# Optimization experiments

Hardware: AMD Instinct MI355X
Metric: run time of the kernel (lower is better)

Reference implementation:

```python
import jax, jax.numpy as jnp
import numpy as np

B = 4            # batches in the sparse tensor
N_PER = 250_000  # occupied voxels per batch item
L = 200          # voxel grid extent per axis
C = 64           # in_channels == out_channels (SE block forces equality)
K = 27           # 3x3x3 kernel offsets
BN_EPS = 1e-5


def _build_neighbors():
    """Unique random voxel coords per batch; kernel map [27, N] (-1 = missing)."""
    rng = np.random.default_rng(0)
    lins, keys = [], []
    for b in range(B):
        lin = np.sort(rng.choice(L ** 3, N_PER, replace=False))
        lins.append(lin)
        keys.append(b * (L ** 3) + lin)
    lin = np.concatenate(lins)
    keys = np.concatenate(keys)          # globally sorted (batch-major)
    bidx = np.repeat(np.arange(B), N_PER)
    x, y, z = lin // (L * L), (lin // L) % L, lin % L
    nbr = np.full((K, B * N_PER), -1, np.int32)
    k = 0
    for dx in (-1, 0, 1):
        for dy in (-1, 0, 1):
            for dz in (-1, 0, 1):
                nx, ny, nz = x + dx, y + dy, z + dz
                inb = (nx >= 0) & (nx < L) & (ny >= 0) & (ny < L) & (nz >= 0) & (nz < L)
                nkey = bidx * (L ** 3) + (nx * L + ny) * L + nz
                pos = np.searchsorted(keys, nkey)
                pos_c = np.clip(pos, 0, keys.size - 1)
                found = inb & (keys[pos_c] == nkey)
                nbr[k] = np.where(found, pos_c, -1).astype(np.int32)
                k += 1
    return nbr, bidx.astype(np.int32)


def setup_inputs() -> dict:
    key = jax.random.key(0)
    ks = jax.random.split(key, 8)
    nbr, bidx = _build_neighbors()
    N = B * N_PER
    s = 1.0 / np.sqrt(K * C)  # fan-in scale for 3x3x3 sparse conv
    R = C // 4                # SE reduction = 4
    return {
        "feats": jax.random.normal(ks[0], (N, C), jnp.float32),
        "neighbor_idx": jnp.asarray(nbr),
        "batch_idx": jnp.asarray(bidx),
        "w_fc1": jax.random.normal(ks[1], (C, R), jnp.float32) / np.sqrt(C),
        "b_fc1": jnp.zeros((R,), jnp.float32),
        "w_fc2": jax.random.normal(ks[2], (R, C), jnp.float32) / np.sqrt(R),
        "b_fc2": jnp.zeros((C,), jnp.float32),
        "w_conv1": jax.random.normal(ks[3], (K, C, C), jnp.float32) * s,
        "bn_gamma": jnp.ones((C,), jnp.float32),
        "bn_beta": jnp.zeros((C,), jnp.float32),
        "bn_mean": jax.random.normal(ks[4], (C,), jnp.float32) * 0.1,
        "bn_var": jax.random.uniform(ks[5], (C,), jnp.float32, 0.5, 1.5),
        "w_conv2": jax.random.normal(ks[6], (K, C, C), jnp.float32) * s,
        "b_conv2": jnp.zeros((C,), jnp.float32),
    }


def _sparse_conv(feats, W, nbr):
    """Minkowski conv: for each offset k, gather neighbor feats, matmul, accumulate."""
    def body(acc, kw):
        idx, Wk = kw                                  # idx: [N], Wk: [Cin, Cout]
        g = jnp.where((idx >= 0)[:, None], feats[jnp.maximum(idx, 0)], 0.0)
        return acc + g @ Wk, None
    acc0 = jnp.zeros((feats.shape[0], W.shape[2]), feats.dtype)
    out, _ = jax.lax.scan(body, acc0, (nbr, W))
    return out


def reference(feats, neighbor_idx, batch_idx, w_fc1, b_fc1, w_fc2, b_fc2,
              w_conv1, bn_gamma, bn_beta, bn_mean, bn_var, w_conv2, b_conv2):
    # SE block: global average pool per batch -> fc -> sigmoid -> broadcast mul
    counts = jax.ops.segment_sum(jnp.ones((feats.shape[0], 1), feats.dtype),
                                 batch_idx, num_segments=B)
    pooled = jax.ops.segment_sum(feats, batch_idx, num_segments=B) / counts  # [B, C]
    h = jax.nn.relu(pooled @ w_fc1 + b_fc1)
    gate = jax.nn.sigmoid(h @ w_fc2 + b_fc2)          # [B, C]
    y = feats * gate[batch_idx]                        # MinkowskiBroadcastMultiplication
    # conv(no bias) -> BN (inference stats) -> ReLU -> conv(+bias)
    h = _sparse_conv(y, w_conv1, neighbor_idx)
    h = (h - bn_mean) * (bn_gamma * jax.lax.rsqrt(bn_var + BN_EPS)) + bn_beta
    h = jax.nn.relu(h)
    return _sparse_conv(h, w_conv2, neighbor_idx) + b_conv2
```

## Files before the change

### kernel.cpp

```cpp
#include <hip/hip_runtime.h>

#define C  64
#define KK 27
#define BB 4

#define PAIR_CAP 1250000
#define KSTRIDE  40960
#define SEGPK    (KSTRIDE / 128)
#define NJ       26

__global__ __launch_bounds__(256) void init_ws(float* ws) {
  int t = blockIdx.x * 256 + threadIdx.x;
  if (t < 1024) ws[t] = 0.f;
}

__global__ __launch_bounds__(256) void pool_kernel(
    const float4* __restrict__ x4, const int* __restrict__ bidx,
    float* __restrict__ pooled, float* __restrict__ counts, int N)
{
  int t = threadIdx.x;
  int g = t & 15;
  int rowInBlk = t >> 4;
  int lane = t & 63, wv = t >> 6;
  float4 acc[BB];
#pragma unroll
  for (int b = 0; b < BB; ++b) acc[b] = make_float4(0.f, 0.f, 0.f, 0.f);
  int cnt[BB] = {0, 0, 0, 0};
  for (int n = blockIdx.x * 16 + rowInBlk; n < N; n += gridDim.x * 16) {
    int b = bidx[n];
    float4 v = x4[((size_t)n << 4) + g];
    if (b == 0)      { acc[0].x += v.x; acc[0].y += v.y; acc[0].z += v.z; acc[0].w += v.w; }
    else if (b == 1) { acc[1].x += v.x; acc[1].y += v.y; acc[1].z += v.z; acc[1].w += v.w; }
    else if (b == 2) { acc[2].x += v.x; acc[2].y += v.y; acc[2].z += v.z; acc[2].w += v.w; }
    else             { acc[3].x += v.x; acc[3].y += v.y; acc[3].z += v.z; acc[3].w += v.w; }
    if (g == 0) {
      if (b == 0) cnt[0]++; else if (b == 1) cnt[1]++;
      else if (b == 2) cnt[2]++; else cnt[3]++;
    }
  }
#pragma unroll
  for (int b = 0; b < BB; ++b) {
    acc[b].x += __shfl_xor(acc[b].x, 16); acc[b].y += __shfl_xor(acc[b].y, 16);
    acc[b].z += __shfl_xor(acc[b].z, 16); acc[b].w += __shfl_xor(acc[b].w, 16);
    acc[b].x += __shfl_xor(acc[b].x, 32); acc[b].y += __shfl_xor(acc[b].y, 32);
    acc[b].z += __shfl_xor(acc[b].z, 32); acc[b].w += __shfl_xor(acc[b].w, 32);
    cnt[b] += __shfl_xor(cnt[b], 16);
    cnt[b] += __shfl_xor(cnt[b], 32);
  }
  __shared__ float red[4][BB][16][4];
  __shared__ int cred[4][BB];
  if (lane < 16) {
#pragma unroll
    for (int b = 0; b < BB; ++b) {
      red[wv][b][lane][0] = acc[b].x; red[wv][b][lane][1] = acc[b].y;
      red[wv][b][lane][2] = acc[b].z; red[wv][b][lane][3] = acc[b].w;
    }
    if (lane == 0) {
#pragma unroll
      for (int b = 0; b < BB; ++b) cred[wv][b] = cnt[b];
    }
  }
  __syncthreads();
  {
    int b = t >> 6, rem = t & 63;
    int gg = rem >> 2, comp = rem & 3;
    float s = red[0][b][gg][comp] + red[1][b][gg][comp] +
              red[2][b][gg][comp] + red[3][b][gg][comp];
    if (s != 0.f) atomicAdd(&pooled[b * C + (gg << 2) + comp], s);
  }
  if (t < BB) {
    int s = cred[0][t] + cred[1][t] + cred[2][t] + cred[3][t];
    if (s) atomicAdd(&counts[t], (float)s);
  }
}

__global__ __launch_bounds__(256) void gate_kernel(
    const float* __restrict__ pooled, const float* __restrict__ counts,
    const float* __restrict__ w_fc1, const float* __restrict__ b_fc1,
    const float* __restrict__ w_fc2, const float* __restrict__ b_fc2,
    const float* __restrict__ bn_gamma, const float* __restrict__ bn_beta,
    const float* __restrict__ bn_mean, const float* __restrict__ bn_var,
    float* __restrict__ gate, float* __restrict__ bnscale, float* __restrict__ bnshift)
{
  __shared__ float mean[BB * C];
  __shared__ float hh[BB * 16];
  int t = threadIdx.x;
  { int b = t >> 6; mean[t] = pooled[t] / counts[b]; }
  __syncthreads();
  if (t < BB * 16) {
    int b = t >> 4, r = t & 15;
    float s = b_fc1[r];
    for (int c = 0; c < C; ++c) s += mean[b * C + c] * w_fc1[c * 16 + r];
    hh[t] = fmaxf(s, 0.f);
  }
  __syncthreads();
  {
    int b = t >> 6, c = t & 63;
    float s = b_fc2[c];
    for (int r = 0; r < 16; ++r) s += hh[b * 16 + r] * w_fc2[r * 64 + c];
    gate[t] = 1.f / (1.f + expf(-s));
  }
  if (t < C) {
    float sc = bn_gamma[t] * rsqrtf(bn_var[t] + 1e-5f);
    bnscale[t] = sc;
    bnshift[t] = bn_beta[t] - bn_mean[t] * sc;
  }
}

__global__ __launch_bounds__(256) void fill_pairs(
    const int* __restrict__ nbr, int* __restrict__ cursor,
    int* __restrict__ pairs, int N)
{
  __shared__ int wc[4][NJ];
  __shared__ int wb[4][NJ];
  int t = threadIdx.x, wv = t >> 6, lane = t & 63;
  int n = blockIdx.x * 256 + t;
  bool act = n < N;
  int v[NJ];
#pragma unroll
  for (int j = 0; j < NJ; ++j) {
    int k = j + (j >= 13);
    v[j] = act ? nbr[(size_t)k * N + n] : -1;
    unsigned long long m = __ballot(v[j] >= 0);
    if (lane == 0) wc[wv][j] = __popcll(m);
  }
  __syncthreads();
  if (t < NJ) {
    int c0 = wc[0][t], c1 = wc[1][t], c2 = wc[2][t], c3 = wc[3][t];
    int tot = c0 + c1 + c2 + c3;
    int b = tot ? atomicAdd(&cursor[t], tot) : 0;
    wb[0][t] = b; wb[1][t] = b + c0; wb[2][t] = b + c0 + c1; wb[3][t] = b + c0 + c1 + c2;
  }
  __syncthreads();
  unsigned long long lt = (1ull << lane) - 1ull;
#pragma unroll
  for (int j = 0; j < NJ; ++j) {
    bool val = v[j] >= 0;
    unsigned long long m = __ballot(val);
    if (!val) continue;
    int pos = wb[wv][j] + __popcll(m & lt);
    if (pos < KSTRIDE) {
      int slot = j * KSTRIDE + pos;
      pairs[slot * 2]     = v[j];
      pairs[slot * 2 + 1] = n;
    }
  }
}

__device__ __forceinline__ void gemm_micro2(const float* Al, const float* Wl,
                                            int rowBase, int coBase, float acc[2][8])
{
#pragma unroll
  for (int i = 0; i < 2; ++i)
#pragma unroll
    for (int j = 0; j < 8; ++j) acc[i][j] = 0.f;
#pragma unroll 4
  for (int ci = 0; ci < 64; ci += 4) {
    float av[2][4];
    *(float4*)av[0] = *(const float4*)&Al[(rowBase    ) * 68 + ci];
    *(float4*)av[1] = *(const float4*)&Al[(rowBase + 8) * 68 + ci];
#pragma unroll
    for (int q = 0; q < 4; ++q) {
      float w8[8];
      *(float4*)&w8[0] = *(const float4*)&Wl[(ci + q) * 64 + coBase];
      *(float4*)&w8[4] = *(const float4*)&Wl[(ci + q) * 64 + coBase + 4];
#pragma unroll
      for (int i = 0; i < 2; ++i)
#pragma unroll
        for (int j = 0; j < 8; ++j)
          acc[i][j] = fmaf(av[i][q], w8[j], acc[i][j]);
    }
  }
}

template <int MODE>
__global__ __launch_bounds__(512) void scatter_k(
    const float* __restrict__ x, const float* __restrict__ Wfull,
    const int* __restrict__ pairs, const int* __restrict__ kcnt,
    const float* __restrict__ bnA, const float* __restrict__ bnB,
    const int* __restrict__ bidx, float* __restrict__ out)
{
  __shared__ float Wl[4096];
  __shared__ float Al[128 * 68];
  __shared__ int Sl[128], Dl[128];
  int j = blockIdx.x / SEGPK;
  int off = (blockIdx.x - j * SEGPK) << 7;
  int pCnt = min(128, kcnt[j] - off);
  if (pCnt <= 0) return;
  int k = j + (j >= 13);
  int t = threadIdx.x;
  int pBase = j * KSTRIDE + off;
  if (t < 128) {
    int s = -1, d = -1;
    if (t < pCnt) { s = pairs[(pBase + t) << 1]; d = pairs[((pBase + t) << 1) | 1]; }
    Sl[t] = s; Dl[t] = d;
  }
  const float* Ws = Wfull + ((size_t)k << 12);
  for (int i = t; i < 4096; i += 512) Wl[i] = Ws[i];
  __syncthreads();
  int rr = t >> 4, c4 = (t & 15) << 2;
  float4 a4, b4;
  if (MODE == 2) { a4 = *(const float4*)&bnA[c4]; b4 = *(const float4*)&bnB[c4]; }
  float4 tv[4];
#pragma unroll
  for (int it = 0; it < 4; ++it) {
    int r = (it << 5) + rr;
    float4 v = make_float4(0.f, 0.f, 0.f, 0.f);
    int src = Sl[r];
    if (src >= 0) {
      v = *(const float4*)(x + ((size_t)src << 6) + c4);
      if (MODE == 1) {
        const float* g = bnA + (bidx[src] << 6) + c4;
        v.x *= g[0]; v.y *= g[1]; v.z *= g[2]; v.w *= g[3];
      } else {
        v.x = fmaxf(fmaf(v.x, a4.x, b4.x), 0.f);
        v.y = fmaxf(fmaf(v.y, a4.y, b4.y), 0.f);
        v.z = fmaxf(fmaf(v.z, a4.z, b4.z), 0.f);
        v.w = fmaxf(fmaf(v.w, a4.w, b4.w), 0.f);
      }
    }
    tv[it] = v;
  }
#pragma unroll
  for (int it = 0; it < 4; ++it) {
    int r = (it << 5) + rr;
    *(float4*)&Al[r * 68 + c4] = tv[it];
  }
  __syncthreads();
  int wv = t >> 6, lane = t & 63, pg = lane >> 3, cg = lane & 7;
  int rowBase = (wv << 4) + pg, coBase = cg << 3;
  float acc[2][8];
  gemm_micro2(Al, Wl, rowBase, coBase, acc);
  __syncthreads();
#pragma unroll
  for (int i = 0; i < 2; ++i) {
    int r = rowBase + (i << 3);
    *(float4*)&Al[r * 68 + coBase]     = *(const float4*)&acc[i][0];
    *(float4*)&Al[r * 68 + coBase + 4] = *(const float4*)&acc[i][4];
  }
  __syncthreads();
  int w0 = wv << 4;
  for (int r2 = 0; r2 < 16; ++r2) {
    int r = w0 + r2;
    int d = Dl[r];
    if (d < 0) continue;
    float val = Al[r * 68 + lane];
    unsafeAtomicAdd(&out[((size_t)d << 6) + lane], val);
  }
}

template <int MODE>
__global__ __launch_bounds__(512) void center_epi(
    const float* __restrict__ x, const float* __restrict__ Wfull,
    const float* __restrict__ gate, const int* __restrict__ bidx,
    const float* __restrict__ bnA, const float* __restrict__ bnB,
    const float* __restrict__ bias, float* __restrict__ out, int N)
{
  __shared__ float Wl[4096];
  __shared__ float Al[128 * 68];
  int t = threadIdx.x;
  int n0 = blockIdx.x << 7;
  int pCnt = min(128, N - n0);
  const float* Ws = Wfull + ((size_t)13 << 12);
  for (int i = t; i < 4096; i += 512) Wl[i] = Ws[i];
  int rr = t >> 4, c4 = (t & 15) << 2;
  float4 a4, b4;
  if (MODE == 1) { a4 = *(const float4*)&bnA[c4]; b4 = *(const float4*)&bnB[c4]; }
  float4 tv[4];
#pragma unroll
  for (int it = 0; it < 4; ++it) {
    int r = (it << 5) + rr;
    float4 v = make_float4(0.f, 0.f, 0.f, 0.f);
    if (r < pCnt) {
      int n = n0 + r;
      v = *(const float4*)(x + ((size_t)n << 6) + c4);
      if (MODE == 0) {
        const float* g = gate + (bidx[n] << 6) + c4;
        v.x *= g[0]; v.y *= g[1]; v.z *= g[2]; v.w *= g[3];
      } else {
        v.x = fmaxf(fmaf(v.x, a4.x, b4.x), 0.f);
        v.y = fmaxf(fmaf(v.y, a4.y, b4.y), 0.f);
        v.z = fmaxf(fmaf(v.z, a4.z, b4.z), 0.f);
        v.w = fmaxf(fmaf(v.w, a4.w, b4.w), 0.f);
      }
    }
    tv[it] = v;
  }
#pragma unroll
  for (int it = 0; it < 4; ++it) {
    int r = (it << 5) + rr;
    *(float4*)&Al[r * 68 + c4] = tv[it];
  }
  __syncthreads();
  int wv = t >> 6, lane = t & 63, pg = lane >> 3, cg = lane & 7;
  int rowBase = (wv << 4) + pg, coBase = cg << 3;
  float acc[2][8];
  gemm_micro2(Al, Wl, rowBase, coBase, acc);
  float4 bb0, bb1;
  if (MODE == 1) { bb0 = *(const float4*)&bias[coBase]; bb1 = *(const float4*)&bias[coBase + 4]; }
#pragma unroll
  for (int i = 0; i < 2; ++i) {
    int r = rowBase + (i << 3);
    if (r < pCnt) {
      size_t o = (((size_t)(n0 + r)) << 6) + coBase;
      float4 r0, r1;
      if (MODE == 0) {
        r0 = make_float4(acc[i][0], acc[i][1], acc[i][2], acc[i][3]);
        r1 = make_float4(acc[i][4], acc[i][5], acc[i][6], acc[i][7]);
      } else {
        r0 = make_float4(acc[i][0] + bb0.x, acc[i][1] + bb0.y,
                         acc[i][2] + bb0.z, acc[i][3] + bb0.w);
        r1 = make_float4(acc[i][4] + bb1.x, acc[i][5] + bb1.y,
                         acc[i][6] + bb1.z, acc[i][7] + bb1.w);
      }
      *(float4*)&out[o]     = r0;
      *(float4*)&out[o + 4] = r1;
    }
  }
}

__global__ __launch_bounds__(256) void scale_w1(
    const float* __restrict__ w1, const float* __restrict__ gate,
    float* __restrict__ w1g)
{
  int b = blockIdx.x & 3, k = blockIdx.x >> 2;
  const float* src = w1 + ((size_t)k << 12);
  float* dst = w1g + (((size_t)(b * KK + k)) << 12);
  const float* g = gate + (b << 6);
  for (int it = 0; it < 16; ++it) {
    int pos = it * 256 + threadIdx.x;
    int ci = pos >> 6;
    dst[pos] = g[ci] * src[pos];
  }
}

template <int MODE>
__global__ __launch_bounds__(256) void spconv_kernel(
    const float* __restrict__ x, const int* __restrict__ nbr,
    const int* __restrict__ bidx, const float* __restrict__ W,
    const float* __restrict__ ep_a, const float* __restrict__ ep_b,
    float* __restrict__ out, int N)
{
  int wid = (int)((blockIdx.x * 256u + threadIdx.x) >> 6);
  if (wid >= N) return;
  int lane = threadIdx.x & 63;
  int n = __builtin_amdgcn_readfirstlane(wid);
  const float* Wb = W;
  if (MODE == 0) {
    int b = __builtin_amdgcn_readfirstlane(bidx[n]);
    Wb += (size_t)b * (KK * C * C);
  }
  float acc = 0.f;
#pragma unroll 1
  for (int k = 0; k < KK; ++k) {
    int idx = __builtin_amdgcn_readfirstlane(nbr[(size_t)k * N + n]);
    if (idx < 0) continue;
    const float* xr = x + ((size_t)idx << 6);
    const float* wr = Wb + (k << 12) + lane;
#pragma unroll
    for (int ci = 0; ci < C; ++ci) acc = fmaf(xr[ci], wr[ci << 6], acc);
  }
  float r;
  if (MODE == 0) r = fmaxf(fmaf(acc, ep_a[lane], ep_b[lane]), 0.f);
  else           r = acc + ep_b[lane];
  out[((size_t)n << 6) + lane] = r;
}

extern "C" void kernel_launch(void* const* d_in, const int* in_sizes, int n_in,
                              void* d_out, int out_size, void* d_ws, size_t ws_size,
                              hipStream_t stream) {
  const float* feats   = (const float*)d_in[0];
  const int*   nbr     = (const int*)  d_in[1];
  const int*   bidx    = (const int*)  d_in[2];
  const float* w_fc1   = (const float*)d_in[3];
  const float* b_fc1   = (const float*)d_in[4];
  const float* w_fc2   = (const float*)d_in[5];
  const float* b_fc2   = (const float*)d_in[6];
  const float* w_conv1 = (const float*)d_in[7];
  const float* bn_gamma= (const float*)d_in[8];
  const float* bn_beta = (const float*)d_in[9];
  const float* bn_mean = (const float*)d_in[10];
  const float* bn_var  = (const float*)d_in[11];
  const float* w_conv2 = (const float*)d_in[12];
  const float* b_conv2 = (const float*)d_in[13];

  int N = in_sizes[0] / C;
  float* ws      = (float*)d_ws;
  float* pooled  = ws;
  float* counts  = ws + 256;
  float* gate    = ws + 260;
  float* bnscale = ws + 516;
  float* bnshift = ws + 580;
  float* out     = (float*)d_out;

  size_t need = ((size_t)16384 + 2ull * PAIR_CAP + (size_t)N * C) * 4ull;

  if (ws_size >= need) {
    int* cursor = (int*)(ws + 698);
    int* pairs  = (int*)(ws + 16384);
    float* h    = ws + 16384 + 2ull * PAIR_CAP;

    hipLaunchKernelGGL(init_ws, dim3(4), dim3(256), 0, stream, ws);
    hipLaunchKernelGGL(pool_kernel, dim3(1024), dim3(256), 0, stream,
                       (const float4*)feats, bidx, pooled, counts, N);
    hipLaunchKernelGGL(gate_kernel, dim3(1), dim3(256), 0, stream,
                       pooled, counts, w_fc1, b_fc1, w_fc2, b_fc2,
                       bn_gamma, bn_beta, bn_mean, bn_var, gate, bnscale, bnshift);
    hipLaunchKernelGGL(fill_pairs, dim3((N + 255) / 256), dim3(256), 0, stream,
                       nbr, cursor, pairs, N);
    hipLaunchKernelGGL((center_epi<0>), dim3((N + 127) / 128), dim3(512), 0, stream,
                       feats, w_conv1, gate, bidx, nullptr, nullptr, nullptr, h, N);
    hipLaunchKernelGGL((scatter_k<1>), dim3(NJ * SEGPK), dim3(512), 0, stream,
                       feats, w_conv1, pairs, cursor, gate, nullptr, bidx, h);
    hipLaunchKernelGGL((center_epi<1>), dim3((N + 127) / 128), dim3(512), 0, stream,
                       h, w_conv2, nullptr, nullptr, bnscale, bnshift, b_conv2, out, N);
    hipLaunchKernelGGL((scatter_k<2>), dim3(NJ * SEGPK), dim3(512), 0, stream,
                       h, w_conv2, pairs, cursor, bnscale, bnshift, nullptr, out);
  } else {
    float* w1g = ws + 1024;
    float* h   = ws + 1024 + BB * KK * C * C;
    hipLaunchKernelGGL(init_ws, dim3(4), dim3(256), 0, stream, ws);
    hipLaunchKernelGGL(pool_kernel, dim3(1024), dim3(256), 0, stream,
                       (const float4*)feats, bidx, pooled, counts, N);
    hipLaunchKernelGGL(gate_kernel, dim3(1), dim3(256), 0, stream,
                       pooled, counts, w_fc1, b_fc1, w_fc2, b_fc2,
                       bn_gamma, bn_beta, bn_mean, bn_var, gate, bnscale, bnshift);
    hipLaunchKernelGGL(scale_w1, dim3(KK * BB), dim3(256), 0, stream,
                       w_conv1, gate, w1g);
    hipLaunchKernelGGL((spconv_kernel<0>), dim3((N + 3) / 4), dim3(256), 0, stream,
                       feats, nbr, bidx, w1g, bnscale, bnshift, h, N);
    hipLaunchKernelGGL((spconv_kernel<1>), dim3((N + 3) / 4), dim3(256), 0, stream,
                       h, nbr, bidx, w_conv2, nullptr, b_conv2, out, N);
  }
}
```

Before: 855.7 us.

## Use fp16 MFMA for per-offset GEMMs with pre-packed half weights

Replaces the scalar FP32 FMA micro-GEMM in the scatter and center kernels with fp16 16x16x32 MFMA instructions. A new w_pack kernel converts both conv weight sets to fp16 in the MFMA B-operand lane layout, so blocks read weights straight from global memory instead of staging them in LDS. Activations are staged in LDS as fp16, which halves the shared-memory footprint. In exchange the GEMM inputs lose precision (fp16 with fp32 accumulate), and the dominant atomic scatter cost is left unchanged.

```diff
diff --git a/kernel.cpp b/kernel.cpp
--- a/kernel.cpp
+++ b/kernel.cpp
@@ -4,10 +4,15 @@
 #define KK 27
 #define BB 4
 
-#define PAIR_CAP 1250000
+typedef _Float16 h4 __attribute__((ext_vector_type(4)));
+typedef _Float16 h8 __attribute__((ext_vector_type(8)));
+typedef float    f4 __attribute__((ext_vector_type(4)));
+
 #define KSTRIDE  40960
 #define SEGPK    (KSTRIDE / 128)
 #define NJ       26
+#define PAIRS_OFF 114688
+#define H_OFF    (PAIRS_OFF + 2 * NJ * KSTRIDE)
 
 __global__ __launch_bounds__(256) void init_ws(float* ws) {
   int t = blockIdx.x * 256 + threadIdx.x;
@@ -107,6 +112,23 @@
   }
 }
 
+__global__ __launch_bounds__(256) void w_pack(
+    const float* __restrict__ W1, const float* __restrict__ W2,
+    _Float16* __restrict__ Wf1, _Float16* __restrict__ Wf2)
+{
+  int kk = blockIdx.x;
+  const float* src = (kk < KK) ? (W1 + ((size_t)kk << 12)) : (W2 + ((size_t)(kk - KK) << 12));
+  _Float16* dst = (kk < KK) ? (Wf1 + ((size_t)kk << 12)) : (Wf2 + ((size_t)(kk - KK) << 12));
+  int t = threadIdx.x;
+  for (int e = 0; e < 16; ++e) {
+    int idx = e * 256 + t;
+    int ci = idx >> 6, co = idx & 63;
+    int kt = ci >> 5, i = ci & 7, lh = (ci >> 3) & 3, ct = co >> 4, col = co & 15;
+    int lane = lh * 16 + col;
+    dst[((kt * 4 + ct) * 64 + lane) * 8 + i] = (_Float16)src[idx];
+  }
+}
+
 __global__ __launch_bounds__(256) void fill_pairs(
     const int* __restrict__ nbr, int* __restrict__ cursor,
     int* __restrict__ pairs, int N)
@@ -147,42 +169,35 @@
   }
 }
 
-__device__ __forceinline__ void gemm_micro2(const float* Al, const float* Wl,
-                                            int rowBase, int coBase, float acc[2][8])
-{
-#pragma unroll
-  for (int i = 0; i < 2; ++i)
-#pragma unroll
-    for (int j = 0; j < 8; ++j) acc[i][j] = 0.f;
-#pragma unroll 4
-  for (int ci = 0; ci < 64; ci += 4) {
-    float av[2][4];
-    *(float4*)av[0] = *(const float4*)&Al[(rowBase    ) * 68 + ci];
-    *(float4*)av[1] = *(const float4*)&Al[(rowBase + 8) * 68 + ci];
-#pragma unroll
-    for (int q = 0; q < 4; ++q) {
-      float w8[8];
-      *(float4*)&w8[0] = *(const float4*)&Wl[(ci + q) * 64 + coBase];
-      *(float4*)&w8[4] = *(const float4*)&Wl[(ci + q) * 64 + coBase + 4];
-#pragma unroll
-      for (int i = 0; i < 2; ++i)
-#pragma unroll
-        for (int j = 0; j < 8; ++j)
-          acc[i][j] = fmaf(av[i][q], w8[j], acc[i][j]);
-    }
+__device__ __forceinline__ void mfma_tile(const _Float16* Af, const h8* Wb,
+                                          int wv, int lane, f4 acc[4])
+{
+  int arow = (wv << 4) + (lane & 15);
+  int koff = (lane >> 4) << 3;
+  h8 a0 = *(const h8*)&Af[arow * 72 + koff];
+  h8 a1 = *(const h8*)&Af[arow * 72 + 32 + koff];
+#pragma unroll
+  for (int ct = 0; ct < 4; ++ct) {
+    h8 b0 = Wb[ct * 64 + lane];
+    h8 b1 = Wb[(4 + ct) * 64 + lane];
+    f4 c = {0.f, 0.f, 0.f, 0.f};
+    c = __builtin_amdgcn_mfma_f32_16x16x32_f16(a0, b0, c, 0, 0, 0);
+    c = __builtin_amdgcn_mfma_f32_16x16x32_f16(a1, b1, c, 0, 0, 0);
+    acc[ct] = c;
   }
 }
 
 template <int MODE>
 __global__ __launch_bounds__(512) void scatter_k(
-    const float* __restrict__ x, const float* __restrict__ Wfull,
+    const float* __restrict__ x, const _Float16* __restrict__ Wf,
     const int* __restrict__ pairs, const int* __restrict__ kcnt,
     const float* __restrict__ bnA, const float* __restrict__ bnB,
     const int* __restrict__ bidx, float* __restrict__ out)
 {
-  __shared__ float Wl[4096];
-  __shared__ float Al[128 * 68];
   __shared__ int Sl[128], Dl[128];
+  __shared__ __align__(16) char uni[128 * 68 * 4];
+  _Float16* Af = (_Float16*)uni;
+  float* Ol = (float*)uni;
   int j = blockIdx.x / SEGPK;
   int off = (blockIdx.x - j * SEGPK) << 7;
   int pCnt = min(128, kcnt[j] - off);
@@ -195,8 +210,6 @@
     if (t < pCnt) { s = pairs[(pBase + t) << 1]; d = pairs[((pBase + t) << 1) | 1]; }
     Sl[t] = s; Dl[t] = d;
   }
-  const float* Ws = Wfull + ((size_t)k << 12);
-  for (int i = t; i < 4096; i += 512) Wl[i] = Ws[i];
   __syncthreads();
   int rr = t >> 4, c4 = (t & 15) << 2;
   float4 a4, b4;
@@ -224,45 +237,44 @@
 #pragma unroll
   for (int it = 0; it < 4; ++it) {
     int r = (it << 5) + rr;
-    *(float4*)&Al[r * 68 + c4] = tv[it];
-  }
-  __syncthreads();
-  int wv = t >> 6, lane = t & 63, pg = lane >> 3, cg = lane & 7;
-  int rowBase = (wv << 4) + pg, coBase = cg << 3;
-  float acc[2][8];
-  gemm_micro2(Al, Wl, rowBase, coBase, acc);
-  __syncthreads();
-#pragma unroll
-  for (int i = 0; i < 2; ++i) {
-    int r = rowBase + (i << 3);
-    *(float4*)&Al[r * 68 + coBase]     = *(const float4*)&acc[i][0];
-    *(float4*)&Al[r * 68 + coBase + 4] = *(const float4*)&acc[i][4];
-  }
+    h4 hv = { (_Float16)tv[it].x, (_Float16)tv[it].y, (_Float16)tv[it].z, (_Float16)tv[it].w };
+    *(h4*)&Af[r * 72 + c4] = hv;
+  }
+  __syncthreads();
+  int wv = t >> 6, lane = t & 63;
+  f4 acc[4];
+  mfma_tile(Af, (const h8*)(Wf + ((size_t)k << 12)), wv, lane, acc);
+  __syncthreads();
+  int orow0 = (wv << 4) + ((lane >> 4) << 2);
+  int ocol = lane & 15;
+#pragma unroll
+  for (int ct = 0; ct < 4; ++ct)
+#pragma unroll
+    for (int rg = 0; rg < 4; ++rg)
+      Ol[(orow0 + rg) * 68 + ct * 16 + ocol] = acc[ct][rg];
   __syncthreads();
   int w0 = wv << 4;
   for (int r2 = 0; r2 < 16; ++r2) {
     int r = w0 + r2;
     int d = Dl[r];
     if (d < 0) continue;
-    float val = Al[r * 68 + lane];
+    float val = Ol[r * 68 + lane];
     unsafeAtomicAdd(&out[((size_t)d << 6) + lane], val);
   }
 }
 
 template <int MODE>
 __global__ __launch_bounds__(512) void center_epi(
-    const float* __restrict__ x, const float* __restrict__ Wfull,
+    const float* __restrict__ x, const _Float16* __restrict__ Wf,
     const float* __restrict__ gate, const int* __restrict__ bidx,
     const float* __restrict__ bnA, const float* __restrict__ bnB,
     const float* __restrict__ bias, float* __restrict__ out, int N)
 {
-  __shared__ float Wl[4096];
-  __shared__ float Al[128 * 68];
+  __shared__ __align__(16) char uni[128 * 72 * 2];
+  _Float16* Af = (_Float16*)uni;
   int t = threadIdx.x;
   int n0 = blockIdx.x << 7;
   int pCnt = min(128, N - n0);
-  const float* Ws = Wfull + ((size_t)13 << 12);
-  for (int i = t; i < 4096; i += 512) Wl[i] = Ws[i];
   int rr = t >> 4, c4 = (t & 15) << 2;
   float4 a4, b4;
   if (MODE == 1) { a4 = *(const float4*)&bnA[c4]; b4 = *(const float4*)&bnB[c4]; }
@@ -289,32 +301,23 @@
 #pragma unroll
   for (int it = 0; it < 4; ++it) {
     int r = (it << 5) + rr;
-    *(float4*)&Al[r * 68 + c4] = tv[it];
-  }
-  __syncthreads();
-  int wv = t >> 6, lane = t & 63, pg = lane >> 3, cg = lane & 7;
-  int rowBase = (wv << 4) + pg, coBase = cg << 3;
-  float acc[2][8];
-  gemm_micro2(Al, Wl, rowBase, coBase, acc);
-  float4 bb0, bb1;
-  if (MODE == 1) { bb0 = *(const float4*)&bias[coBase]; bb1 = *(const float4*)&bias[coBase + 4]; }
-#pragma unroll
-  for (int i = 0; i < 2; ++i) {
-    int r = rowBase + (i << 3);
-    if (r < pCnt) {
-      size_t o = (((size_t)(n0 + r)) << 6) + coBase;
-      float4 r0, r1;
-      if (MODE == 0) {
-        r0 = make_float4(acc[i][0], acc[i][1], acc[i][2], acc[i][3]);
-        r1 = make_float4(acc[i][4], acc[i][5], acc[i][6], acc[i][7]);
-      } else {
-        r0 = make_float4(acc[i][0] + bb0.x, acc[i][1] + bb0.y,
-                         acc[i][2] + bb0.z, acc[i][3] + bb0.w);
-        r1 = make_float4(acc[i][4] + bb1.x, acc[i][5] + bb1.y,
-                         acc[i][6] + bb1.z, acc[i][7] + bb1.w);
-      }
-      *(float4*)&out[o]     = r0;
-      *(float4*)&out[o + 4] = r1;
+    h4 hv = { (_Float16)tv[it].x, (_Float16)tv[it].y, (_Float16)tv[it].z, (_Float16)tv[it].w };
+    *(h4*)&Af[r * 72 + c4] = hv;
+  }
+  __syncthreads();
+  int wv = t >> 6, lane = t & 63;
+  f4 acc[4];
+  mfma_tile(Af, (const h8*)(Wf + ((size_t)13 << 12)), wv, lane, acc);
+  int orow0 = (wv << 4) + ((lane >> 4) << 2);
+  int ocol = lane & 15;
+#pragma unroll
+  for (int ct = 0; ct < 4; ++ct) {
+    float bv = (MODE == 1) ? bias[ct * 16 + ocol] : 0.f;
+#pragma unroll
+    for (int rg = 0; rg < 4; ++rg) {
+      int r = orow0 + rg;
+      if (r < pCnt)
+        out[(((size_t)(n0 + r)) << 6) + ct * 16 + ocol] = acc[ct][rg] + bv;
     }
   }
 }
@@ -393,12 +396,14 @@
   float* bnshift = ws + 580;
   float* out     = (float*)d_out;
 
-  size_t need = ((size_t)16384 + 2ull * PAIR_CAP + (size_t)N * C) * 4ull;
+  size_t need = ((size_t)H_OFF + (size_t)N * C) * 4ull;
 
   if (ws_size >= need) {
     int* cursor = (int*)(ws + 698);
-    int* pairs  = (int*)(ws + 16384);
-    float* h    = ws + 16384 + 2ull * PAIR_CAP;
+    _Float16* Wf1 = (_Float16*)(ws + 1024);
+    _Float16* Wf2 = (_Float16*)(ws + 56320);
+    int* pairs  = (int*)(ws + PAIRS_OFF);
+    float* h    = ws + H_OFF;
 
     hipLaunchKernelGGL(init_ws, dim3(4), dim3(256), 0, stream, ws);
     hipLaunchKernelGGL(pool_kernel, dim3(1024), dim3(256), 0, stream,
@@ -406,16 +411,18 @@
     hipLaunchKernelGGL(gate_kernel, dim3(1), dim3(256), 0, stream,
                        pooled, counts, w_fc1, b_fc1, w_fc2, b_fc2,
                        bn_gamma, bn_beta, bn_mean, bn_var, gate, bnscale, bnshift);
+    hipLaunchKernelGGL(w_pack, dim3(2 * KK), dim3(256), 0, stream,
+                       w_conv1, w_conv2, Wf1, Wf2);
     hipLaunchKernelGGL(fill_pairs, dim3((N + 255) / 256), dim3(256), 0, stream,
                        nbr, cursor, pairs, N);
     hipLaunchKernelGGL((center_epi<0>), dim3((N + 127) / 128), dim3(512), 0, stream,
-                       feats, w_conv1, gate, bidx, nullptr, nullptr, nullptr, h, N);
+                       feats, Wf1, gate, bidx, nullptr, nullptr, nullptr, h, N);
     hipLaunchKernelGGL((scatter_k<1>), dim3(NJ * SEGPK), dim3(512), 0, stream,
-                       feats, w_conv1, pairs, cursor, gate, nullptr, bidx, h);
+                       feats, Wf1, pairs, cursor, gate, nullptr, bidx, h);
     hipLaunchKernelGGL((center_epi<1>), dim3((N + 127) / 128), dim3(512), 0, stream,
-                       h, w_conv2, nullptr, nullptr, bnscale, bnshift, b_conv2, out, N);
+                       h, Wf2, nullptr, nullptr, bnscale, bnshift, b_conv2, out, N);
     hipLaunchKernelGGL((scatter_k<2>), dim3(NJ * SEGPK), dim3(512), 0, stream,
-                       h, w_conv2, pairs, cursor, bnscale, bnshift, nullptr, out);
+                       h, Wf2, pairs, cursor, bnscale, bnshift, nullptr, out);
   } else {
     float* w1g = ws + 1024;
     float* h   = ws + 1024 + BB * KK * C * C;
```

New measurement: 721.1 us. 15.7% less time.
